# Optimization experiments

Hardware: AMD Instinct MI355X
Metric: run time of the kernel (lower is better)

## Reference

```python
import jax, jax.numpy as jnp
import numpy as np

# 8 fixed 3x3 shift-and-subtract kernels (center -1, one neighbor +1)
_KERNELS = np.array([
    [[1, 0, 0], [0, -1, 0], [0, 0, 0]],
    [[0, 1, 0], [0, -1, 0], [0, 0, 0]],
    [[0, 0, 1], [0, -1, 0], [0, 0, 0]],
    [[0, 0, 0], [1, -1, 0], [0, 0, 0]],
    [[0, 0, 0], [0, -1, 1], [0, 0, 0]],
    [[0, 0, 0], [0, -1, 0], [1, 0, 0]],
    [[0, 0, 0], [0, -1, 0], [0, 1, 0]],
    [[0, 0, 0], [0, -1, 0], [0, 0, 1]],
], dtype=np.float32)  # [8,3,3]


def contrast_depth_conv(x):
    # x: [B, H, W] single-channel depth map.
    # torch does groups=8 depthwise conv on the input broadcast to 8 channels,
    # which is identical to a 1->8 channel VALID conv with the 8 kernels.
    w = jnp.asarray(_KERNELS)[:, None, :, :]  # [8,1,3,3] OIHW
    y = jax.lax.conv_general_dilated(
        x[:, None, :, :],  # [B,1,H,W] NCHW
        w,
        window_strides=(1, 1),
        padding='VALID',
        dimension_numbers=('NCHW', 'OIHW', 'NCHW'),
    )
    return y  # [B, 8, H-2, W-2]


def setup_inputs() -> dict:
    key = jax.random.key(0)
    k1, k2 = jax.random.split(key)
    B, H, W = 16384, 32, 32
    out = jax.random.normal(k1, (B, H, W), dtype=jnp.float32)
    label = jax.random.normal(k2, (B, H, W), dtype=jnp.float32)
    return {"out": out, "label": label}


def reference(out, label):
    c_out = contrast_depth_conv(out)      # [B,8,30,30]
    c_label = contrast_depth_conv(label)  # [B,8,30,30]
    diff = c_out - c_label
    return jnp.mean(diff * diff)
```

## Files before the change

### kernel.cpp

```cpp
#include <hip/hip_runtime.h>


#define THREADS 256
#define IPB 8

__global__ __launch_bounds__(THREADS, 2) void cdl_partial(
    const float* __restrict__ outp,
    const float* __restrict__ labp,
    float* __restrict__ partial,
    int nimg)
{
    const int t = threadIdx.x;
    float acc = 0.f;

    if (t < 225) {
        const int qy = t / 15, qx = t - qy * 15;
        const long long base = (long long)blockIdx.x * IPB * 1024
                             + (2 * qy) * 32 + 2 * qx;
        const float* ob = outp + base;
        const float* lb = labp + base;
        const int n = (nimg - blockIdx.x * IPB < IPB) ? (nimg - blockIdx.x * IPB) : IPB;

        #pragma unroll 2
        for (int i = 0; i < n; ++i) {
            const float* o = ob + i * 1024;
            const float* l = lb + i * 1024;
            float2 ov[4][2], lv[4][2];
            #pragma unroll
            for (int r = 0; r < 4; ++r) {
                ov[r][0] = *(const float2*)(o + r * 32);
                ov[r][1] = *(const float2*)(o + r * 32 + 2);
                lv[r][0] = *(const float2*)(l + r * 32);
                lv[r][1] = *(const float2*)(l + r * 32 + 2);
            }
            float dd[4][4];
            #pragma unroll
            for (int r = 0; r < 4; ++r) {
                dd[r][0] = ov[r][0].x - lv[r][0].x;
                dd[r][1] = ov[r][0].y - lv[r][0].y;
                dd[r][2] = ov[r][1].x - lv[r][1].x;
                dd[r][3] = ov[r][1].y - lv[r][1].y;
            }
            #pragma unroll
            for (int cy = 1; cy <= 2; ++cy) {
                #pragma unroll
                for (int cx = 1; cx <= 2; ++cx) {
                    const float c = dd[cy][cx];
                    #pragma unroll
                    for (int ny = -1; ny <= 1; ++ny) {
                        #pragma unroll
                        for (int nx = -1; nx <= 1; ++nx) {
                            if (ny == 0 && nx == 0) continue;
                            const float v = dd[cy + ny][cx + nx] - c;
                            acc += v * v;
                        }
                    }
                }
            }
        }
    }

    #pragma unroll
    for (int off = 32; off; off >>= 1) acc += __shfl_down(acc, off, 64);
    __shared__ float red[4];
    const int lane = t & 63, wid = t >> 6;
    if (lane == 0) red[wid] = acc;
    __syncthreads();
    if (t == 0) partial[blockIdx.x] = red[0] + red[1] + red[2] + red[3];
}

__global__ __launch_bounds__(THREADS) void cdl_final(
    const float* __restrict__ partial,
    float* __restrict__ out,
    int np,
    float inv_count)
{
    __shared__ float red[THREADS / 64];
    const int t = threadIdx.x;
    float acc = 0.f;
    for (int i = t; i < np; i += THREADS) acc += partial[i];
    #pragma unroll
    for (int off = 32; off; off >>= 1) acc += __shfl_down(acc, off, 64);
    if ((t & 63) == 0) red[t >> 6] = acc;
    __syncthreads();
    if (t == 0) out[0] = (red[0] + red[1] + red[2] + red[3]) * inv_count;
}

extern "C" void kernel_launch(void* const* d_in, const int* in_sizes, int n_in,
                              void* d_out, int out_size, void* d_ws, size_t ws_size,
                              hipStream_t stream) {
    const float* outp = (const float*)d_in[0];
    const float* labp = (const float*)d_in[1];
    float* partial = (float*)d_ws;
    const int nimg = in_sizes[0] / 1024;
    const int nblocks = (nimg + IPB - 1) / IPB;
    const float inv_count = 1.0f / ((float)nimg * 8.0f * 900.0f);

    cdl_partial<<<nblocks, THREADS, 0, stream>>>(outp, labp, partial, nimg);
    cdl_final<<<1, THREADS, 0, stream>>>(partial, (float*)d_out, nblocks, inv_count);
}
```

Before: 28.54 us.

## Stage images through LDS with async global_load_lds triple buffering and fuse final reduction

Replaces direct per-thread overlapping global loads with coalesced 16-byte global_load_lds transfers into a triple-buffered LDS ring. Each block processes 4 batches of 2 images, prefetching two batches ahead and gating compute with explicit vmcnt waits and barriers. The separate final-reduction kernel is folded in through an atomic last-block pattern, which needs a memset of the counter. This trades the extra launch and redundant overlapping global loads for LDS traffic, barrier overhead, and lower occupancy from 48KB of LDS per block.

Result: slower. 85.73 us (+200.4%).

```diff
diff --git a/kernel.cpp b/kernel.cpp
--- a/kernel.cpp
+++ b/kernel.cpp
@@ -2,45 +2,66 @@
 
 
 #define THREADS 256
-#define IPB 8
+#define NBUF 3
+#define BI 2
+#define NB 4
 
-__global__ __launch_bounds__(THREADS, 2) void cdl_partial(
+#define GLOAD_LDS(g, l) __builtin_amdgcn_global_load_lds( \
+    (const __attribute__((address_space(1))) void*)(g),   \
+    (__attribute__((address_space(3))) void*)(l), 16, 0, 0)
+
+__global__ __launch_bounds__(THREADS) void cdl_fused(
     const float* __restrict__ outp,
     const float* __restrict__ labp,
     float* __restrict__ partial,
-    int nimg)
+    int* __restrict__ counter,
+    float* __restrict__ out,
+    int nimg, float inv_count)
 {
+    __shared__ float lds[NBUF][2][BI * 1024];
+    __shared__ float red[4];
+
     const int t = threadIdx.x;
+    const int lane = t & 63, wid = t >> 6;
+    const int img0 = blockIdx.x * (NB * BI);
+
     float acc = 0.f;
 
-    if (t < 225) {
-        const int qy = t / 15, qx = t - qy * 15;
-        const long long base = (long long)blockIdx.x * IPB * 1024
-                             + (2 * qy) * 32 + 2 * qx;
-        const float* ob = outp + base;
-        const float* lb = labp + base;
-        const int n = (nimg - blockIdx.x * IPB < IPB) ? (nimg - blockIdx.x * IPB) : IPB;
+    auto stage = [&](int bf, int bb) {
+        const int ia = min(img0 + bb * BI,     nimg - 1);
+        const int ib = min(img0 + bb * BI + 1, nimg - 1);
+        const long long g0 = (long long)(wid < 2 ? ia : ib) * 1024
+                           + (wid & 1) * 512 + lane * 4;
+        const float* go = outp + g0;
+        const float* gl = labp + g0;
+        float* lo = &lds[bf][0][wid * 512];
+        float* ll = &lds[bf][1][wid * 512];
+        GLOAD_LDS(go,       lo);
+        GLOAD_LDS(go + 256, lo + 256);
+        GLOAD_LDS(gl,       ll);
+        GLOAD_LDS(gl + 256, ll + 256);
+    };
 
-        #pragma unroll 2
-        for (int i = 0; i < n; ++i) {
-            const float* o = ob + i * 1024;
-            const float* l = lb + i * 1024;
-            float2 ov[4][2], lv[4][2];
-            #pragma unroll
-            for (int r = 0; r < 4; ++r) {
-                ov[r][0] = *(const float2*)(o + r * 32);
-                ov[r][1] = *(const float2*)(o + r * 32 + 2);
-                lv[r][0] = *(const float2*)(l + r * 32);
-                lv[r][1] = *(const float2*)(l + r * 32 + 2);
-            }
+    auto compute = [&](int bf, int bb) {
+        #pragma unroll
+        for (int it = 0; it < 2; ++it) {
+            const int tt = it * 256 + t;
+            const int tk = (tt < 450) ? tt : 0;
+            const int img = tk / 225, q = tk - img * 225;
+            const bool act = (tt < 450) && (img0 + bb * BI + img < nimg);
+            const int qy = q / 15, qx = q - qy * 15;
+            const int bw = img * 1024 + qy * 64 + qx * 2;
             float dd[4][4];
             #pragma unroll
             for (int r = 0; r < 4; ++r) {
-                dd[r][0] = ov[r][0].x - lv[r][0].x;
-                dd[r][1] = ov[r][0].y - lv[r][0].y;
-                dd[r][2] = ov[r][1].x - lv[r][1].x;
-                dd[r][3] = ov[r][1].y - lv[r][1].y;
+                const float2 o0 = *(const float2*)&lds[bf][0][bw + 32 * r];
+                const float2 o1 = *(const float2*)&lds[bf][0][bw + 32 * r + 2];
+                const float2 l0 = *(const float2*)&lds[bf][1][bw + 32 * r];
+                const float2 l1 = *(const float2*)&lds[bf][1][bw + 32 * r + 2];
+                dd[r][0] = o0.x - l0.x; dd[r][1] = o0.y - l0.y;
+                dd[r][2] = o1.x - l1.x; dd[r][3] = o1.y - l1.y;
             }
+            float sub = 0.f;
             #pragma unroll
             for (int cy = 1; cy <= 2; ++cy) {
                 #pragma unroll
@@ -52,38 +73,50 @@
                         for (int nx = -1; nx <= 1; ++nx) {
                             if (ny == 0 && nx == 0) continue;
                             const float v = dd[cy + ny][cx + nx] - c;
-                            acc += v * v;
+                            sub += v * v;
                         }
                     }
                 }
             }
+            acc += act ? sub : 0.f;
         }
+    };
+
+    stage(0, 0);
+    stage(1, 1);
+    for (int b = 0; b < NB; ++b) {
+        if (b + 2 < NB) stage((b + 2) % NBUF, b + 2);
+        if (b + 2 < NB)      asm volatile("s_waitcnt vmcnt(8)" ::: "memory");
+        else if (b + 1 < NB) asm volatile("s_waitcnt vmcnt(4)" ::: "memory");
+        else                 asm volatile("s_waitcnt vmcnt(0)" ::: "memory");
+        asm volatile("s_barrier" ::: "memory");
+        compute(b % NBUF, b);
+        asm volatile("s_barrier" ::: "memory");
     }
 
     #pragma unroll
     for (int off = 32; off; off >>= 1) acc += __shfl_down(acc, off, 64);
-    __shared__ float red[4];
-    const int lane = t & 63, wid = t >> 6;
     if (lane == 0) red[wid] = acc;
     __syncthreads();
-    if (t == 0) partial[blockIdx.x] = red[0] + red[1] + red[2] + red[3];
-}
+    if (t == 0) {
+        partial[blockIdx.x] = red[0] + red[1] + red[2] + red[3];
+        __threadfence();
+    }
 
-__global__ __launch_bounds__(THREADS) void cdl_final(
-    const float* __restrict__ partial,
-    float* __restrict__ out,
-    int np,
-    float inv_count)
-{
-    __shared__ float red[THREADS / 64];
-    const int t = threadIdx.x;
-    float acc = 0.f;
-    for (int i = t; i < np; i += THREADS) acc += partial[i];
-    #pragma unroll
-    for (int off = 32; off; off >>= 1) acc += __shfl_down(acc, off, 64);
-    if ((t & 63) == 0) red[t >> 6] = acc;
+    __shared__ int is_last;
+    if (t == 0) is_last = (atomicAdd(counter, 1) == (int)gridDim.x - 1) ? 1 : 0;
     __syncthreads();
-    if (t == 0) out[0] = (red[0] + red[1] + red[2] + red[3]) * inv_count;
+    if (is_last) {
+        __threadfence();
+        float a = 0.f;
+        const int nb = (int)gridDim.x;
+        for (int i = t; i < nb; i += THREADS) a += partial[i];
+        #pragma unroll
+        for (int off = 32; off; off >>= 1) a += __shfl_down(a, off, 64);
+        if (lane == 0) red[wid] = a;
+        __syncthreads();
+        if (t == 0) out[0] = (red[0] + red[1] + red[2] + red[3]) * inv_count;
+    }
 }
 
 extern "C" void kernel_launch(void* const* d_in, const int* in_sizes, int n_in,
@@ -91,11 +124,14 @@
                               hipStream_t stream) {
     const float* outp = (const float*)d_in[0];
     const float* labp = (const float*)d_in[1];
-    float* partial = (float*)d_ws;
     const int nimg = in_sizes[0] / 1024;
-    const int nblocks = (nimg + IPB - 1) / IPB;
+    const int nblocks = (nimg + NB * BI - 1) / (NB * BI);
     const float inv_count = 1.0f / ((float)nimg * 8.0f * 900.0f);
 
-    cdl_partial<<<nblocks, THREADS, 0, stream>>>(outp, labp, partial, nimg);
-    cdl_final<<<1, THREADS, 0, stream>>>(partial, (float*)d_out, nblocks, inv_count);
+    int* counter = (int*)d_ws;
+    float* partial = (float*)d_ws + 64;
+    hipMemsetAsync(counter, 0, sizeof(int), stream);
+
+    cdl_fused<<<nblocks, THREADS, 0, stream>>>(outp, labp, partial, counter,
+                                               (float*)d_out, nimg, inv_count);
 }
```

## Enlarge per-thread tile to 6x6 outputs with 8x8 halo, flatten image-thread mapping

Applied to the files above, without the earlier changes.

Each thread now computes a 6x6 block of output centers from an 8x8 register tile, instead of a 2x2 block from a 4x4 tile. Threads map directly to (image, tile) pairs across the whole grid, 25 tiles per image, replacing the 8-images-per-block loop. The larger tile cuts halo re-reads from 4x to about 1.8x and removes idle lanes, and four split accumulators shorten the add chain. In exchange each thread holds many more registers, and loads within a wavefront stride 24 bytes apart, which may hurt coalescing and occupancy.

After: 28.92 us. No clear change (+1.3%).

```diff
diff --git a/kernel.cpp b/kernel.cpp
--- a/kernel.cpp
+++ b/kernel.cpp
@@ -2,7 +2,6 @@
 
 
 #define THREADS 256
-#define IPB 8
 
 __global__ __launch_bounds__(THREADS, 2) void cdl_partial(
     const float* __restrict__ outp,
@@ -10,55 +9,63 @@
     float* __restrict__ partial,
     int nimg)
 {
-    const int t = threadIdx.x;
-    float acc = 0.f;
+    const int t  = threadIdx.x;
+    const int tg = blockIdx.x * THREADS + t;
+    const int img = tg / 25;
+    const int tau = tg - img * 25;
+    const int ty = tau / 5, tx = tau - ty * 5;
 
-    if (t < 225) {
-        const int qy = t / 15, qx = t - qy * 15;
-        const long long base = (long long)blockIdx.x * IPB * 1024
-                             + (2 * qy) * 32 + 2 * qx;
-        const float* ob = outp + base;
-        const float* lb = labp + base;
-        const int n = (nimg - blockIdx.x * IPB < IPB) ? (nimg - blockIdx.x * IPB) : IPB;
+    float a0 = 0.f, a1 = 0.f, a2 = 0.f, a3 = 0.f;
 
-        #pragma unroll 2
-        for (int i = 0; i < n; ++i) {
-            const float* o = ob + i * 1024;
-            const float* l = lb + i * 1024;
-            float2 ov[4][2], lv[4][2];
+    if (img < nimg) {
+        const long long fb = (long long)img * 1024 + (6 * ty) * 32 + 6 * tx;
+        const float2* ob = (const float2*)(outp + fb);
+        const float2* lb = (const float2*)(labp + fb);
+
+        float2 ov[8][4], lv[8][4];
+        #pragma unroll
+        for (int r = 0; r < 8; ++r) {
             #pragma unroll
-            for (int r = 0; r < 4; ++r) {
-                ov[r][0] = *(const float2*)(o + r * 32);
-                ov[r][1] = *(const float2*)(o + r * 32 + 2);
-                lv[r][0] = *(const float2*)(l + r * 32);
-                lv[r][1] = *(const float2*)(l + r * 32 + 2);
+            for (int c = 0; c < 4; ++c) ov[r][c] = ob[r * 16 + c];
+        }
+        #pragma unroll
+        for (int r = 0; r < 8; ++r) {
+            #pragma unroll
+            for (int c = 0; c < 4; ++c) lv[r][c] = lb[r * 16 + c];
+        }
+
+        float d[8][8];
+        #pragma unroll
+        for (int r = 0; r < 8; ++r) {
+            #pragma unroll
+            for (int c = 0; c < 4; ++c) {
+                d[r][2 * c]     = ov[r][c].x - lv[r][c].x;
+                d[r][2 * c + 1] = ov[r][c].y - lv[r][c].y;
             }
-            float dd[4][4];
+        }
+
+        #pragma unroll
+        for (int cy = 1; cy <= 6; ++cy) {
             #pragma unroll
-            for (int r = 0; r < 4; ++r) {
-                dd[r][0] = ov[r][0].x - lv[r][0].x;
-                dd[r][1] = ov[r][0].y - lv[r][0].y;
-                dd[r][2] = ov[r][1].x - lv[r][1].x;
-                dd[r][3] = ov[r][1].y - lv[r][1].y;
-            }
-            #pragma unroll
-            for (int cy = 1; cy <= 2; ++cy) {
-                #pragma unroll
-                for (int cx = 1; cx <= 2; ++cx) {
-                    const float c = dd[cy][cx];
-                    #pragma unroll
-                    for (int ny = -1; ny <= 1; ++ny) {
-                        #pragma unroll
-                        for (int nx = -1; nx <= 1; ++nx) {
-                            if (ny == 0 && nx == 0) continue;
-                            const float v = dd[cy + ny][cx + nx] - c;
-                            acc += v * v;
-                        }
-                    }
-                }
+            for (int cx = 1; cx <= 6; ++cx) {
+                const float c = d[cy][cx];
+                float s = 0.f, v;
+                v = d[cy - 1][cx - 1] - c; s += v * v;
+                v = d[cy - 1][cx    ] - c; s += v * v;
+                v = d[cy - 1][cx + 1] - c; s += v * v;
+                v = d[cy    ][cx - 1] - c; s += v * v;
+                v = d[cy    ][cx + 1] - c; s += v * v;
+                v = d[cy + 1][cx - 1] - c; s += v * v;
+                v = d[cy + 1][cx    ] - c; s += v * v;
+                v = d[cy + 1][cx + 1] - c; s += v * v;
+                const int k = (cy * 6 + cx) & 3;
+                if (k == 0) a0 += s; else if (k == 1) a1 += s;
+                else if (k == 2) a2 += s; else a3 += s;
             }
         }
     }
+
+    float acc = (a0 + a1) + (a2 + a3);
 
     #pragma unroll
     for (int off = 32; off; off >>= 1) acc += __shfl_down(acc, off, 64);
@@ -93,7 +100,8 @@
     const float* labp = (const float*)d_in[1];
     float* partial = (float*)d_ws;
     const int nimg = in_sizes[0] / 1024;
-    const int nblocks = (nimg + IPB - 1) / IPB;
+    const long long ntask = (long long)nimg * 25;
+    const int nblocks = (int)((ntask + THREADS - 1) / THREADS);
     const float inv_count = 1.0f / ((float)nimg * 8.0f * 900.0f);
 
     cdl_partial<<<nblocks, THREADS, 0, stream>>>(outp, labp, partial, nimg);
```
